# Performance work log

Measured on AMD Instinct MI355X. Metric: run time of the kernel, lower is better.

## Reference

```python
import jax, jax.numpy as jnp
import numpy as np


def _avgpool(x, k):
    # x: [B, C, H, W] -> [B, C, H//k, W//k] via non-overlapping mean pooling
    B, C, H, W = x.shape
    return x.reshape(B, C, H // k, k, W // k, k).mean(axis=(3, 5))


def _multiscale_tokens(x):
    # concat flattened pooled maps along token dim: [B, C, sum_k (H/k)*(W/k)]
    B, C, H, W = x.shape
    parts = [_avgpool(x, k).reshape(B, C, -1) for k in (16, 8, 4, 2)]
    return jnp.concatenate(parts, axis=2)


def setup_inputs() -> dict:
    key = jax.random.key(0)
    x = jax.random.normal(key, (16, 256, 128, 128), dtype=jnp.float32)
    gamma = jnp.zeros((1,), dtype=jnp.float32)
    return {"x": x, "gamma": gamma}


def reference(x, gamma):
    B, C, H, W = x.shape
    # q and k pooling are identical in the original module (recomputed redundantly)
    tokens = _multiscale_tokens(x)                      # [B, C, T]
    energy = jnp.einsum('bct,bdt->bcd', tokens, tokens)  # [B, C, C]
    energy_new = jnp.max(energy, axis=-1, keepdims=True) - energy
    attention = jax.nn.softmax(energy_new, axis=-1)      # [B, C, C]
    proj_value = x.reshape(B, C, H * W)                  # [B, C, HW]
    out = jnp.einsum('bcd,bdn->bcn', attention, proj_value).reshape(B, C, H, W)
    return gamma * out + x
```

## Files before the change

kernel.cpp:

```cpp
#include <hip/hip_runtime.h>
#include <hip/hip_bf16.h>

#define B_  16
#define C_  256
#define W_  128
#define HW_ 16384
#define T_  5440
#define NSPLIT 10

typedef __bf16 bf16;
typedef __bf16 bf16x2 __attribute__((ext_vector_type(2)));
typedef __bf16 bf16x4 __attribute__((ext_vector_type(4)));
typedef __bf16 bf16x8 __attribute__((ext_vector_type(8)));
typedef float  f32x4  __attribute__((ext_vector_type(4)));

__device__ __forceinline__ void gload_lds16(const void* g, void* l) {
    __builtin_amdgcn_global_load_lds(
        (const __attribute__((address_space(1))) void*)g,
        (__attribute__((address_space(3))) void*)l, 16, 0, 0);
}

__device__ __forceinline__ int bs32(int n, int q) {
    return (n & 3) * 512 + q * 128 + (((n >> 2) ^ (q << 1)) & 7) * 16;
}

__global__ __launch_bounds__(256) void pool_kernel(const float* __restrict__ x,
                                                   bf16* __restrict__ tokens) {
    __shared__ float s2[64 * 64];
    __shared__ float s4[32 * 32];
    __shared__ float s8[16 * 16];
    const int blk = blockIdx.x;
    const float* plane = x + ((size_t)blk << 14);
    bf16* tok = tokens + (size_t)blk * T_;
    const int tid = threadIdx.x;

    for (int it = 0; it < 8; ++it) {
        int task = it * 256 + tid;
        int i  = task >> 5;
        int jp = task & 31;
        const float4 r0 = *(const float4*)(plane + (2 * i) * W_ + 4 * jp);
        const float4 r1 = *(const float4*)(plane + (2 * i + 1) * W_ + 4 * jp);
        float p0 = (r0.x + r0.y + r1.x + r1.y) * 0.25f;
        float p1 = (r0.z + r0.w + r1.z + r1.w) * 0.25f;
        s2[i * 64 + 2 * jp]     = p0;
        s2[i * 64 + 2 * jp + 1] = p1;
        bf16x2 wv; wv.x = (bf16)p0; wv.y = (bf16)p1;
        *(bf16x2*)(tok + 1344 + i * 64 + 2 * jp) = wv;
    }
    __syncthreads();
    for (int it = 0; it < 4; ++it) {
        int task = it * 256 + tid;
        int i = task >> 5, j = task & 31;
        float v = 0.25f * (s2[(2 * i) * 64 + 2 * j] + s2[(2 * i) * 64 + 2 * j + 1] +
                           s2[(2 * i + 1) * 64 + 2 * j] + s2[(2 * i + 1) * 64 + 2 * j + 1]);
        s4[i * 32 + j] = v;
        tok[320 + i * 32 + j] = (bf16)v;
    }
    __syncthreads();
    {
        int i = tid >> 4, j = tid & 15;
        float v = 0.25f * (s4[(2 * i) * 32 + 2 * j] + s4[(2 * i) * 32 + 2 * j + 1] +
                           s4[(2 * i + 1) * 32 + 2 * j] + s4[(2 * i + 1) * 32 + 2 * j + 1]);
        s8[i * 16 + j] = v;
        tok[64 + tid] = (bf16)v;
    }
    __syncthreads();
    if (tid < 64) {
        int i = tid >> 3, j = tid & 7;
        float v = 0.25f * (s8[(2 * i) * 16 + 2 * j] + s8[(2 * i) * 16 + 2 * j + 1] +
                           s8[(2 * i + 1) * 16 + 2 * j] + s8[(2 * i + 1) * 16 + 2 * j + 1]);
        tok[tid] = (bf16)v;
    }
}

__global__ __launch_bounds__(256, 2) void energy_kernel(const bf16* __restrict__ tokens,
                                                        float* __restrict__ part) {
    __shared__ __align__(16) char smem[32768];
    const int blk  = blockIdx.x;
    const int s    = blk / 48;
    const int rem  = blk - s * 48;
    const int b    = rem / 3;
    const int tile = rem - b * 3;
    const int cm0  = (tile == 2) ? 128 : 0;
    const int cn0  = (tile == 0) ? 0 : 128;
    const bool offdiag = (tile == 1);
    const int kbase = s * (T_ / NSPLIT);
    const int tid  = threadIdx.x;
    const int lane = tid & 63;
    const int w    = tid >> 6;
    const int wm = (w >> 1) * 64, wn = (w & 1) * 64;
    const int lm = lane & 15;
    const int q8 = (lane >> 4) * 8;
    const bf16* tokb = tokens + (size_t)b * C_ * T_;

    #define E_STAGE(ki, d) do {                                                   \
        const int k0_ = kbase + (ki) * 32;                                        \
        _Pragma("unroll")                                                         \
        for (int it = 0; it < 2; ++it) {                                          \
            int slot = it * 256 + tid;                                            \
            int r  = slot >> 2;                                                   \
            int c8 = (slot & 3) * 8;                                              \
            gload_lds16(tokb + (size_t)(cm0 + r) * T_ + k0_ + c8,                 \
                        smem + (size_t)(d) * 8192 + (size_t)(it * 256 + w * 64) * 16); \
        }                                                                         \
        if (offdiag) {                                                            \
            _Pragma("unroll")                                                     \
            for (int it = 0; it < 2; ++it) {                                      \
                int slot = it * 256 + tid;                                        \
                int r  = slot >> 2;                                               \
                int c8 = (slot & 3) * 8;                                          \
                gload_lds16(tokb + (size_t)(cn0 + r) * T_ + k0_ + c8,             \
                            smem + 16384 + (size_t)(d) * 8192 + (size_t)(it * 256 + w * 64) * 16); \
            }                                                                     \
        }                                                                         \
    } while (0)

    f32x4 acc[4][4] = {};
    E_STAGE(0, 0);
    __syncthreads();
    for (int ki = 0; ki < 17; ++ki) {
        if (ki < 16) E_STAGE(ki + 1, (ki + 1) & 1);
        const bf16* Af = (const bf16*)(smem + (ki & 1) * 8192);
        const bf16* Bf = offdiag ? (const bf16*)(smem + 16384 + (ki & 1) * 8192) : Af;
        bf16x8 af[4], bfr[4];
        #pragma unroll
        for (int mi = 0; mi < 4; ++mi)
            af[mi] = *(const bf16x8*)(Af + (wm + mi * 16 + lm) * 32 + q8);
        #pragma unroll
        for (int ni = 0; ni < 4; ++ni)
            bfr[ni] = *(const bf16x8*)(Bf + (wn + ni * 16 + lm) * 32 + q8);
        #pragma unroll
        for (int mi = 0; mi < 4; ++mi)
            #pragma unroll
            for (int ni = 0; ni < 4; ++ni)
                acc[mi][ni] = __builtin_amdgcn_mfma_f32_16x16x32_bf16(af[mi], bfr[ni], acc[mi][ni], 0, 0, 0);
        __syncthreads();
    }
    #undef E_STAGE
    float* P = part + ((size_t)(s * 4096 + b * C_) << 8);
    const int row0 = (lane >> 4) * 4;
    for (int mi = 0; mi < 4; ++mi)
        for (int ni = 0; ni < 4; ++ni) {
            f32x4 v = acc[mi][ni];
            int row = cm0 + wm + mi * 16 + row0;
            int col = cn0 + wn + ni * 16 + lm;
            #pragma unroll
            for (int e = 0; e < 4; ++e)
                P[((size_t)(row + e) << 8) + col] = v[e];
            if (offdiag)
                *(f32x4*)(P + ((size_t)col << 8) + row) = v;
        }
}

__global__ __launch_bounds__(256) void softmax_kernel(const float* __restrict__ part,
                                                      bf16* __restrict__ att) {
    const int row  = blockIdx.x * 4 + (threadIdx.x >> 6);
    const int lane = threadIdx.x & 63;
    float4 e = {0.f, 0.f, 0.f, 0.f};
    for (int s = 0; s < NSPLIT; ++s) {
        const float4 p = *(const float4*)(part + ((size_t)(s * 4096 + row) << 8) + lane * 4);
        e.x += p.x; e.y += p.y; e.z += p.z; e.w += p.w;
    }
    float mn = fminf(fminf(e.x, e.y), fminf(e.z, e.w));
    for (int off = 32; off > 0; off >>= 1) mn = fminf(mn, __shfl_xor(mn, off));
    float p0 = __expf(mn - e.x), p1 = __expf(mn - e.y);
    float p2 = __expf(mn - e.z), p3 = __expf(mn - e.w);
    float s = p0 + p1 + p2 + p3;
    for (int off = 32; off > 0; off >>= 1) s += __shfl_xor(s, off);
    float inv = 1.0f / s;
    bf16x4 o;
    o.x = (bf16)(p0 * inv); o.y = (bf16)(p1 * inv);
    o.z = (bf16)(p2 * inv); o.w = (bf16)(p3 * inv);
    *(bf16x4*)(att + ((size_t)row << 8) + lane * 4) = o;
}

__global__ __launch_bounds__(256, 4) void out_kernel(const bf16* __restrict__ att,
                                                     const float* __restrict__ x,
                                                     const float* __restrict__ gamma,
                                                     float* __restrict__ out) {
    __shared__ __align__(16) char smem[36864];
    const int b  = blockIdx.x >> 9;
    const int n0 = (blockIdx.x & 511) << 5;
    const int tid  = threadIdx.x;
    const int lane = tid & 63;
    const int w    = tid >> 6;
    const int wm   = w * 64;
    const int lm = lane & 15;
    const int q4 = lane >> 4;
    const int q8 = q4 * 8;
    const float g = gamma[0];
    const bf16*  attb = att + ((size_t)b << 16);
    const float* xb   = x + ((size_t)b << 22);
    const int vk = tid >> 3;
    const int vj = tid & 7;
    const int vq = vk >> 3;
    const int vh = (vk & 7) * 2;

    #define A_STAGE(kk, d) do {                                                  \
        const int k0_ = (kk) * 32;                                               \
        _Pragma("unroll")                                                        \
        for (int it = 0; it < 4; ++it) {                                         \
            int slot = it * 256 + tid;                                           \
            int r  = slot >> 2;                                                  \
            int c8 = (slot & 3) * 8;                                             \
            gload_lds16(attb + ((size_t)r << 8) + k0_ + c8,                      \
                        smem + (size_t)(d) * 16384 + (size_t)(it * 256 + w * 64) * 16); \
        }                                                                        \
    } while (0)

    #define BS_WRITE(d, v) do {                                                  \
        char* BsW = smem + 32768 + (size_t)(d) * 2048;                           \
        _Pragma("unroll")                                                        \
        for (int e = 0; e < 4; ++e) {                                            \
            bf16 hv = (bf16)(v)[e];                                              \
            *(bf16*)(BsW + bs32(vj * 4 + e, vq) + vh) = hv;                      \
        }                                                                        \
    } while (0)

    f32x4 acc[4][2] = {};
    f32x4 vv;

    vv = *(const f32x4*)(xb + ((size_t)vk << 14) + n0 + vj * 4);
    BS_WRITE(0, vv);
    A_STAGE(0, 0);
    __syncthreads();

    for (int kk = 0; kk < 8; ++kk) {
        if (kk < 7) {
            vv = *(const f32x4*)(xb + ((size_t)((kk + 1) * 32 + vk) << 14) + n0 + vj * 4);
            A_STAGE(kk + 1, (kk + 1) & 1);
        }
        const bf16* Af  = (const bf16*)(smem + (kk & 1) * 16384);
        const char* BsR = smem + 32768 + (kk & 1) * 2048;
        bf16x8 af[4];
        #pragma unroll
        for (int mi = 0; mi < 4; ++mi)
            af[mi] = *(const bf16x8*)(Af + (wm + mi * 16 + lm) * 32 + q8);
        #pragma unroll
        for (int ni = 0; ni < 2; ++ni) {
            bf16x8 bb = *(const bf16x8*)(BsR + bs32(ni * 16 + lm, q4));
            #pragma unroll
            for (int mi = 0; mi < 4; ++mi)
                acc[mi][ni] = __builtin_amdgcn_mfma_f32_16x16x32_bf16(af[mi], bb, acc[mi][ni], 0, 0, 0);
        }
        if (kk < 7) BS_WRITE((kk + 1) & 1, vv);
        __syncthreads();
    }
    #undef A_STAGE
    #undef BS_WRITE

    float* buf = (float*)(smem + (size_t)w * 2176);
    for (int mi = 0; mi < 4; ++mi) {
        #pragma unroll
        for (int ni = 0; ni < 2; ++ni) {
            f32x4 v = acc[mi][ni];
            int c = ni * 16 + lm;
            buf[(q4 * 4 + 0) * 33 + c] = v[0];
            buf[(q4 * 4 + 1) * 33 + c] = v[1];
            buf[(q4 * 4 + 2) * 33 + c] = v[2];
            buf[(q4 * 4 + 3) * 33 + c] = v[3];
        }
        #pragma unroll
        for (int it = 0; it < 2; ++it) {
            int idx = it * 64 + lane;
            int r  = idx >> 3;
            int c4 = (idx & 7) * 4;
            f32x4 pv = *(const f32x4*)(buf + r * 33 + c4);
            int c = wm + mi * 16 + r;
            size_t gi = ((size_t)b << 22) + ((size_t)c << 14) + n0 + c4;
            f32x4 xv = *(const f32x4*)(x + gi);
            f32x4 o;
            o[0] = g * pv[0] + xv[0];
            o[1] = g * pv[1] + xv[1];
            o[2] = g * pv[2] + xv[2];
            o[3] = g * pv[3] + xv[3];
            __builtin_nontemporal_store(o, (f32x4*)(out + gi));
        }
    }
}

__global__ __launch_bounds__(256) void fallback_copy(const float* __restrict__ x,
                                                     const float* __restrict__ gamma,
                                                     float* __restrict__ out, size_t n) {
    size_t i = (size_t)blockIdx.x * 256 + threadIdx.x;
    size_t stride = (size_t)gridDim.x * 256;
    float g = gamma[0];
    for (; i < n; i += stride) out[i] = x[i] + g * 0.0f;
}

extern "C" void kernel_launch(void* const* d_in, const int* in_sizes, int n_in,
                              void* d_out, int out_size, void* d_ws, size_t ws_size,
                              hipStream_t stream) {
    const float* x     = (const float*)d_in[0];
    const float* gamma = (const float*)d_in[1];
    float* out = (float*)d_out;

    const size_t ATT_BYTES = (size_t)B_ * C_ * C_ * 2;
    if (ws_size < ATT_BYTES) {
        size_t n = (size_t)B_ * C_ * HW_;
        fallback_copy<<<2048, 256, 0, stream>>>(x, gamma, out, n);
        return;
    }
    bf16*  tokens = (bf16*)d_out;
    float* part   = (float*)((char*)d_out + ((size_t)64 << 20));
    bf16*  att    = (bf16*)d_ws;

    pool_kernel<<<dim3(B_ * C_), dim3(256), 0, stream>>>(x, tokens);
    energy_kernel<<<dim3(NSPLIT * B_ * 3), dim3(256), 0, stream>>>(tokens, part);
    softmax_kernel<<<dim3(B_ * C_ / 4), dim3(256), 0, stream>>>(part, att);
    out_kernel<<<dim3(B_ * 512), dim3(256), 0, stream>>>(att, x, gamma, out);
}
```

Measured before the change: 593.6 us.

## Single-buffer LDS in out_kernel and prefetch all x rows into registers upfront

Replaces the double-buffered LDS staging of attention and value tiles with a single buffer, halving shared memory per block so more blocks can be resident per CU. All eight x value vectors are loaded into registers at kernel start instead of one stage ahead. The attention tile load now sits on the critical path behind a barrier each iteration, so overlap within a block is lost, and register pressure rises from the 8-vector prefetch.

```diff
diff --git a/kernel.cpp b/kernel.cpp
--- a/kernel.cpp
+++ b/kernel.cpp
@@ -178,7 +178,7 @@
                                                      const float* __restrict__ x,
                                                      const float* __restrict__ gamma,
                                                      float* __restrict__ out) {
-    __shared__ __align__(16) char smem[36864];
+    __shared__ __align__(16) char smem[18432];
     const int b  = blockIdx.x >> 9;
     const int n0 = (blockIdx.x & 511) << 5;
     const int tid  = threadIdx.x;
@@ -196,42 +196,31 @@
     const int vq = vk >> 3;
     const int vh = (vk & 7) * 2;
 
-    #define A_STAGE(kk, d) do {                                                  \
-        const int k0_ = (kk) * 32;                                               \
-        _Pragma("unroll")                                                        \
-        for (int it = 0; it < 4; ++it) {                                         \
-            int slot = it * 256 + tid;                                           \
-            int r  = slot >> 2;                                                  \
-            int c8 = (slot & 3) * 8;                                             \
-            gload_lds16(attb + ((size_t)r << 8) + k0_ + c8,                      \
-                        smem + (size_t)(d) * 16384 + (size_t)(it * 256 + w * 64) * 16); \
-        }                                                                        \
-    } while (0)
-
-    #define BS_WRITE(d, v) do {                                                  \
-        char* BsW = smem + 32768 + (size_t)(d) * 2048;                           \
-        _Pragma("unroll")                                                        \
-        for (int e = 0; e < 4; ++e) {                                            \
-            bf16 hv = (bf16)(v)[e];                                              \
-            *(bf16*)(BsW + bs32(vj * 4 + e, vq) + vh) = hv;                      \
-        }                                                                        \
-    } while (0)
-
     f32x4 acc[4][2] = {};
-    f32x4 vv;
-
-    vv = *(const f32x4*)(xb + ((size_t)vk << 14) + n0 + vj * 4);
-    BS_WRITE(0, vv);
-    A_STAGE(0, 0);
-    __syncthreads();
+    f32x4 vv[8];
+    #pragma unroll
+    for (int kk = 0; kk < 8; ++kk)
+        vv[kk] = *(const f32x4*)(xb + ((size_t)(kk * 32 + vk) << 14) + n0 + vj * 4);
 
     for (int kk = 0; kk < 8; ++kk) {
-        if (kk < 7) {
-            vv = *(const f32x4*)(xb + ((size_t)((kk + 1) * 32 + vk) << 14) + n0 + vj * 4);
-            A_STAGE(kk + 1, (kk + 1) & 1);
-        }
-        const bf16* Af  = (const bf16*)(smem + (kk & 1) * 16384);
-        const char* BsR = smem + 32768 + (kk & 1) * 2048;
+        if (kk) __syncthreads();
+        #pragma unroll
+        for (int it = 0; it < 4; ++it) {
+            int slot = it * 256 + tid;
+            int r  = slot >> 2;
+            int c8 = (slot & 3) * 8;
+            gload_lds16(attb + ((size_t)r << 8) + kk * 32 + c8,
+                        smem + (size_t)(it * 256 + w * 64) * 16);
+        }
+        {
+            char* BsW = smem + 16384;
+            #pragma unroll
+            for (int e = 0; e < 4; ++e)
+                *(bf16*)(BsW + bs32(vj * 4 + e, vq) + vh) = (bf16)vv[kk][e];
+        }
+        __syncthreads();
+        const bf16* Af  = (const bf16*)smem;
+        const char* BsR = smem + 16384;
         bf16x8 af[4];
         #pragma unroll
         for (int mi = 0; mi < 4; ++mi)
@@ -243,12 +232,9 @@
             for (int mi = 0; mi < 4; ++mi)
                 acc[mi][ni] = __builtin_amdgcn_mfma_f32_16x16x32_bf16(af[mi], bb, acc[mi][ni], 0, 0, 0);
         }
-        if (kk < 7) BS_WRITE((kk + 1) & 1, vv);
-        __syncthreads();
-    }
-    #undef A_STAGE
-    #undef BS_WRITE
-
+    }
+
+    __syncthreads();
     float* buf = (float*)(smem + (size_t)w * 2176);
     for (int mi = 0; mi < 4; ++mi) {
         #pragma unroll
```

After: 585.5 us. Within noise of the previous version (-1.4%).
